# Kernel tuning notes

Hardware: AMD Instinct MI355X
Metric: run time of the kernel (lower is better)

The kernel has to match this reference:

```python
import jax, jax.numpy as jnp
import numpy as np

E4M3_MAX = 448.0
IGNORE = -1000.0
ROTARY_BASE = 10000.0


def quant_dequant_e4m3(w):
    """Emulate per-tensor FP8 E4M3 quantize->dequantize (3 mantissa bits, max 448)."""
    amax = jnp.max(jnp.abs(w))
    scale = E4M3_MAX / jnp.maximum(amax, 1e-12)
    v = w * scale
    a = jnp.abs(v)
    # exponent clipped to E4M3 range (min normal exp -6, max 8)
    e = jnp.clip(jnp.floor(jnp.log2(jnp.maximum(a, 1e-30))), -6.0, 8.0)
    step = jnp.exp2(e - 3.0)  # 3 mantissa bits
    q = jnp.clip(jnp.round(v / step) * step, -E4M3_MAX, E4M3_MAX)
    return (q / scale).astype(w.dtype)


def rotary_sin_cos(rotary_dim, n_ctx):
    pos = jnp.arange(n_ctx, dtype=jnp.float32)
    dim = jnp.arange(rotary_dim // 2, dtype=jnp.float32)
    inv_freq = ROTARY_BASE ** (-dim / (rotary_dim / 2))
    ang = pos[:, None] * inv_freq[None, :]            # [n_ctx, rotary_dim//2]
    ang = jnp.concatenate([ang, ang], axis=-1)        # [n_ctx, rotary_dim]
    return jnp.sin(ang), jnp.cos(ang)


def apply_rotary(x, sin, cos, rotary_dim):
    # x: [B, S, H, Dh]; rotate first rotary_dim dims with rotate-half convention
    S = x.shape[1]
    x_rot, x_pass = x[..., :rotary_dim], x[..., rotary_dim:]
    half = rotary_dim // 2
    x_flip = jnp.concatenate([-x_rot[..., half:], x_rot[..., :half]], axis=-1)
    c = cos[:S][None, :, None, :]
    s = sin[:S][None, :, None, :]
    out = x_rot * c + x_flip * s
    return jnp.concatenate([out, x_pass], axis=-1) if rotary_dim < x.shape[-1] else out


def setup_inputs() -> dict:
    key = jax.random.key(0)
    ks = jax.random.split(key, 8)
    B, S, D, H, Dh = 2, 2048, 1024, 16, 64
    return {
        "query_input": jax.random.normal(ks[0], (B, S, D), jnp.float32),
        "key_input": jax.random.normal(ks[1], (B, S, D), jnp.float32),
        "value_input": jax.random.normal(ks[2], (B, S, D), jnp.float32),
        "W_Q": jax.random.normal(ks[3], (H, D, Dh), jnp.float32) * 0.02,
        "W_K": jax.random.normal(ks[4], (H, D, Dh), jnp.float32) * 0.02,
        "W_V": jax.random.normal(ks[5], (H, D, Dh), jnp.float32) * 0.02,
        "W_O": jax.random.normal(ks[6], (H, Dh, D), jnp.float32) * 0.02,
        "b_Q": jnp.zeros((H, Dh), jnp.float32),
        "b_K": jnp.zeros((H, Dh), jnp.float32),
        "b_V": jnp.zeros((H, Dh), jnp.float32),
        "b_O": jnp.zeros((D,), jnp.float32),
    }


def reference(query_input, key_input, value_input, W_Q, W_K, W_V, W_O, b_Q, b_K, b_V, b_O):
    B, S, D = query_input.shape
    H, _, Dh = W_Q.shape
    rotary_dim = Dh
    attn_scale = jnp.sqrt(jnp.asarray(Dh, jnp.float32))

    # FP8-quantized QKV weights/biases (E4M3 quant-dequant emulation)
    Wq = quant_dequant_e4m3(W_Q)
    Wk = quant_dequant_e4m3(W_K)
    Wv = quant_dequant_e4m3(W_V)
    bq = quant_dequant_e4m3(b_Q)
    bk = quant_dequant_e4m3(b_K)
    bv = quant_dequant_e4m3(b_V)

    q = jnp.einsum("bsd,hde->bshe", query_input, Wq) + bq  # [B,S,H,Dh]
    k = jnp.einsum("bsd,hde->bshe", key_input, Wk) + bk
    v = jnp.einsum("bsd,hde->bshe", value_input, Wv) + bv

    sin, cos = rotary_sin_cos(rotary_dim, S)
    q = apply_rotary(q, sin, cos, rotary_dim)
    k = apply_rotary(k, sin, cos, rotary_dim)

    scores = jnp.einsum("bqhe,bkhe->bhqk", q, k) / attn_scale  # [B,H,S,S]
    causal = jnp.tril(jnp.ones((S, S), bool))
    scores = jnp.where(causal[None, None], scores, IGNORE)
    pattern = jax.nn.softmax(scores, axis=-1)

    z = jnp.einsum("bhqk,bkhe->bqhe", pattern, v)             # [B,S,H,Dh]
    out = jnp.einsum("bqhe,hed->bqd", z, W_O) + b_O           # [B,S,D]
    return out
```

## Files before the change

kernel.cpp:

```cpp
#include <hip/hip_runtime.h>
#include <math.h>


typedef __attribute__((ext_vector_type(8))) short bf16x8;
typedef __attribute__((ext_vector_type(16))) float f32x16;
typedef __attribute__((ext_vector_type(4))) float f32x4;
typedef __attribute__((ext_vector_type(4))) float f4;

#define E4M3_MAX 448.0f

__device__ inline float bf2f(ushort u) { return __uint_as_float(((unsigned)u) << 16); }
__device__ inline ushort f2bf(float f) {
  unsigned u = __float_as_uint(f);
  return (ushort)((u + 0x7FFF + ((u >> 16) & 1)) >> 16);
}
__device__ inline unsigned pack2bf(float a, float b) {
  unsigned ua = __float_as_uint(a), ub = __float_as_uint(b);
  return ((ua + 0x8000u) >> 16) | ((ub + 0x8000u) & 0xFFFF0000u);
}

__device__ __forceinline__ void gll16(const ushort* g, ushort* l) {
  __builtin_amdgcn_global_load_lds(
      (const __attribute__((address_space(1))) unsigned int*)g,
      (__attribute__((address_space(3))) unsigned int*)l, 16, 0, 0);
}

__global__ void zero16_kernel(float* p) {
  if (threadIdx.x < 16) p[threadIdx.x] = 0.0f;
}

__global__ __launch_bounds__(256) void amax6_kernel(const float* __restrict__ p0,
                                                    const float* __restrict__ p1,
                                                    const float* __restrict__ p2,
                                                    const float* __restrict__ p3,
                                                    const float* __restrict__ p4,
                                                    const float* __restrict__ p5,
                                                    float* __restrict__ amax) {
  int y = blockIdx.y;
  const float* src = (y == 0) ? p0 : (y == 1) ? p1 : (y == 2) ? p2 : (y == 3) ? p3 : (y == 4) ? p4 : p5;
  int n = (y < 3) ? 1048576 : 1024;
  float m = 0.0f;
  int stride = gridDim.x * 256;
  for (int i = blockIdx.x * 256 + threadIdx.x; i < n; i += stride)
    m = fmaxf(m, fabsf(src[i]));
  #pragma unroll
  for (int off = 32; off > 0; off >>= 1)
    m = fmaxf(m, __shfl_xor(m, off));
  __shared__ float wred[4];
  if ((threadIdx.x & 63) == 0) wred[threadIdx.x >> 6] = m;
  __syncthreads();
  if (threadIdx.x == 0) {
    m = fmaxf(fmaxf(wred[0], wred[1]), fmaxf(wred[2], wred[3]));
    atomicMax((unsigned int*)(amax + y), __float_as_uint(m));
  }
}

__device__ inline float qdq_qval(float w, float amax) {
  float scale = E4M3_MAX / fmaxf(amax, 1e-12f);
  float v = w * scale;
  float a = fmaxf(fabsf(v), 1e-30f);
  int ex;
  (void)frexpf(a, &ex);
  float e = fminf(fmaxf((float)(ex - 1), -6.0f), 8.0f);
  float step = exp2f(e - 3.0f);
  float q = rintf(v / step) * step;
  return fminf(fmaxf(q, -E4M3_MAX), E4M3_MAX);
}

__global__ void qvec3_kernel(const float* __restrict__ b0, const float* __restrict__ b1,
                             const float* __restrict__ b2, const float* __restrict__ amax,
                             float* __restrict__ o0, float* __restrict__ o1,
                             float* __restrict__ o2) {
  int y = blockIdx.y;
  const float* b = (y == 0) ? b0 : (y == 1) ? b1 : b2;
  float* o = (y == 0) ? o0 : (y == 1) ? o1 : o2;
  float am = amax[3 + y];
  int idx = blockIdx.x * blockDim.x + threadIdx.x;
  if (idx < 1024) {
    float q = qdq_qval(b[idx], am);
    o[idx] = q * (fmaxf(am, 1e-12f) * (1.0f / E4M3_MAX));
  }
}

__global__ __launch_bounds__(256) void quant_repack_bt3(const float* __restrict__ W0,
                                                        const float* __restrict__ W1,
                                                        const float* __restrict__ W2,
                                                        const float* __restrict__ amaxp,
                                                        ushort* __restrict__ o0,
                                                        ushort* __restrict__ o1,
                                                        ushort* __restrict__ o2) {
  int z = blockIdx.z;
  const float* W = (z == 0) ? W0 : (z == 1) ? W1 : W2;
  ushort* Bt = (z == 0) ? o0 : (z == 1) ? o1 : o2;
  float amax = amaxp[z];
  __shared__ float tile[64][65];
  int d0 = blockIdx.x * 64, hh = blockIdx.y;
  int tid = threadIdx.x;
  int e = tid & 63, dd = tid >> 6;
  #pragma unroll
  for (int p = 0; p < 16; p++)
    tile[dd + p * 4][e] = W[(size_t)hh * 65536 + (size_t)(d0 + dd + p * 4) * 64 + e];
  __syncthreads();
  int d = tid & 63, ee = tid >> 6;
  #pragma unroll
  for (int p = 0; p < 16; p++) {
    int e2 = ee + p * 4;
    Bt[(size_t)(hh * 64 + e2) * 1024 + d0 + d] = f2bf(qdq_qval(tile[d][e2], amax));
  }
}

__global__ __launch_bounds__(256) void wo_trans(const float* __restrict__ W,
                                               ushort* __restrict__ Bt) {
  __shared__ float tile[64][65];
  int d0 = blockIdx.x * 64, he0 = blockIdx.y * 64;
  int tid = threadIdx.x;
  int dcol = tid & 63, hr = tid >> 6;
  #pragma unroll
  for (int p = 0; p < 16; p++)
    tile[hr + p * 4][dcol] = W[(size_t)(he0 + hr + p * 4) * 1024 + d0 + dcol];
  __syncthreads();
  int hcol = tid & 63, dr = tid >> 6;
  #pragma unroll
  for (int p = 0; p < 16; p++)
    Bt[(size_t)(d0 + dr + p * 4) * 1024 + he0 + hcol] = f2bf(tile[hcol][dr + p * 4]);
}

__global__ __launch_bounds__(256) void cvt3_kernel(const float* __restrict__ i0,
                                                   const float* __restrict__ i1,
                                                   const float* __restrict__ i2,
                                                   ushort* __restrict__ o0,
                                                   ushort* __restrict__ o1,
                                                   ushort* __restrict__ o2) {
  int y = blockIdx.y;
  const float* in = (y == 0) ? i0 : (y == 1) ? i1 : i2;
  ushort* out = (y == 0) ? o0 : (y == 1) ? o1 : o2;
  int i = blockIdx.x * 256 + threadIdx.x;
  f4 v = *(const f4*)(in + (size_t)i * 4);
  uint2 o;
  o.x = (unsigned)f2bf(v[0]) | ((unsigned)f2bf(v[1]) << 16);
  o.y = (unsigned)f2bf(v[2]) | ((unsigned)f2bf(v[3]) << 16);
  *(uint2*)(out + (size_t)i * 4) = o;
}

template <int QUANT, int TN>
__device__ __forceinline__ void gemm_body(const ushort* __restrict__ A,
                                          const ushort* __restrict__ Bt,
                                          const float* __restrict__ bias, float s_inv,
                                          ushort* __restrict__ outb, float* __restrict__ outf,
                                          int bx, int by, ushort* As, ushort* Bs) {
  const int K = 1024, N = 1024;
  const int JF = TN / 32;
  int tid = threadIdx.x;
  int w = tid >> 6, lane = tid & 63, quad = lane >> 4, l16 = lane & 15;
  int wm = w & 1, wn = w >> 1;
  int row0 = by * 128, col0 = bx * TN;
  f32x4 acc[4][4] = {};

  for (int k0 = 0; k0 < K; k0 += 32) {
    __syncthreads();
    {
      int u = tid;
      gll16(&A[(size_t)(row0 + (u >> 2)) * K + k0 + (u & 3) * 8], &As[u * 8]);
      u = tid + 256;
      gll16(&A[(size_t)(row0 + (u >> 2)) * K + k0 + (u & 3) * 8], &As[u * 8]);
      u = tid;
      gll16(&Bt[(size_t)(col0 + (u >> 2)) * K + k0 + (u & 3) * 8], &Bs[u * 8]);
      if (TN == 128) {
        u = tid + 256;
        gll16(&Bt[(size_t)(col0 + (u >> 2)) * K + k0 + (u & 3) * 8], &Bs[u * 8]);
      }
    }
    __syncthreads();
    bf16x8 af[4], bfr[JF];
    #pragma unroll
    for (int i = 0; i < 4; i++)
      af[i] = *(const bf16x8*)&As[(wm * 64 + i * 16 + l16) * 32 + quad * 8];
    #pragma unroll
    for (int j = 0; j < JF; j++)
      bfr[j] = *(const bf16x8*)&Bs[(wn * (TN / 2) + j * 16 + l16) * 32 + quad * 8];
    #pragma unroll
    for (int i = 0; i < 4; i++)
      #pragma unroll
      for (int j = 0; j < JF; j++)
        acc[i][j] = __builtin_amdgcn_mfma_f32_16x16x32_bf16(af[i], bfr[j], acc[i][j], 0, 0, 0);
  }

  #pragma unroll
  for (int j = 0; j < JF; j++) {
    int col = col0 + wn * (TN / 2) + j * 16 + l16;
    float bv = bias[col];
    #pragma unroll
    for (int i = 0; i < 4; i++) {
      int row = row0 + wm * 64 + i * 16 + quad * 4;
      #pragma unroll
      for (int r = 0; r < 4; r++) {
        float v = acc[i][j][r] * s_inv + bv;
        if (QUANT) outb[(size_t)(row + r) * N + col] = f2bf(v);
        else       outf[(size_t)(row + r) * N + col] = v;
      }
    }
  }
}

__global__ __launch_bounds__(256) void gemm3_qkv(const ushort* __restrict__ xq,
                                                 const ushort* __restrict__ xk,
                                                 const ushort* __restrict__ xv,
                                                 const ushort* __restrict__ wq,
                                                 const ushort* __restrict__ wk,
                                                 const ushort* __restrict__ wv,
                                                 const float* __restrict__ bq,
                                                 const float* __restrict__ bk,
                                                 const float* __restrict__ bv,
                                                 const float* __restrict__ amax,
                                                 ushort* __restrict__ oq,
                                                 ushort* __restrict__ ok,
                                                 ushort* __restrict__ ov) {
  __shared__ ushort As[4096], Bs[4096];
  int z = blockIdx.z;
  const ushort* A  = (z == 0) ? xq : (z == 1) ? xk : xv;
  const ushort* Bt = (z == 0) ? wq : (z == 1) ? wk : wv;
  const float* bias = (z == 0) ? bq : (z == 1) ? bk : bv;
  ushort* out = (z == 0) ? oq : (z == 1) ? ok : ov;
  float s_inv = fmaxf(amax[z], 1e-12f) * (1.0f / E4M3_MAX);
  gemm_body<1, 128>(A, Bt, bias, s_inv, out, nullptr, blockIdx.x, blockIdx.y, As, Bs);
}

__global__ __launch_bounds__(256) void gemm_wo(const ushort* __restrict__ A,
                                               const ushort* __restrict__ Bt,
                                               const float* __restrict__ bias,
                                               float* __restrict__ out) {
  __shared__ ushort As[4096], Bs[2048];
  gemm_body<0, 64>(A, Bt, bias, 1.0f, nullptr, out, blockIdx.x, blockIdx.y, As, Bs);
}

__global__ __launch_bounds__(256) void rotary_bf(ushort* qb, ushort* kb) {
  int bs = blockIdx.x;
  int s = bs & 2047;
  int tid = threadIdx.x;
  int e = tid & 63, w = tid >> 6;
  int j = e & 31;
  float inv_freq = exp2f((float)j * (-13.287712379549449f / 32.0f));
  float ang = (float)s * inv_freq;
  float c = cosf(ang), sn = sinf(ang);
  float sgn = (e < 32) ? -1.0f : 1.0f;
  size_t base = (size_t)bs * 1024;
  #pragma unroll
  for (int i = 0; i < 4; i++) {
    int h = w + i * 4;
    size_t idx = base + (size_t)h * 64 + e;
    float x = bf2f(qb[idx]);
    float xp = __shfl_xor(x, 32);
    qb[idx] = f2bf(x * c + sgn * xp * sn);
    float y = bf2f(kb[idx]);
    float yp = __shfl_xor(y, 32);
    kb[idx] = f2bf(y * c + sgn * yp * sn);
  }
}

__global__ __launch_bounds__(256) void v_trans(const ushort* __restrict__ v,
                                              ushort* __restrict__ vT) {
  __shared__ ushort tile[64][72];
  int s0 = blockIdx.x * 64, h = blockIdx.y, b = blockIdx.z;
  int tid = threadIdx.x;
  int e = tid & 63, sr = tid >> 6;
  #pragma unroll
  for (int p = 0; p < 16; p++)
    tile[sr + p * 4][e] = v[(size_t)(b * 2048 + s0 + sr + p * 4) * 1024 + h * 64 + e];
  __syncthreads();
  int sc = tid & 63, er = tid >> 6;
  #pragma unroll
  for (int p = 0; p < 16; p++)
    vT[(size_t)((b * 16 + h) * 64 + er + p * 4) * 2048 + s0 + sc] = tile[sc][er + p * 4];
}

__global__ __launch_bounds__(512, 4) void flash_mfma6(const ushort* __restrict__ qb,
                                                      const ushort* __restrict__ kb,
                                                      const ushort* __restrict__ vT,
                                                      ushort* __restrict__ zb) {
  int h = blockIdx.y, b = blockIdx.z;
  int tid = threadIdx.x;
  int w8 = tid >> 6;
  int g = w8 >> 2;
  int w = w8 & 3;
  int lane = tid & 63, h2 = lane >> 5, l31 = lane & 31;
  __shared__ ushort sbuf[16384 + 18432];
  ushort* Ks = sbuf + g * 4096;
  ushort* Vs = sbuf + 8192 + g * 4096;
  ushort* P2 = sbuf + 16384 + g * 9216;

  const int qrow = w * 32 + l31;
  const float CE = 0.125f;

  const int ts = tid & 255;
  const int u0 = ts, u1 = ts + 256;
  const int r0 = u0 >> 3, c0 = u0 & 7, r1 = u1 >> 3, c1 = u1 & 7;
  const int sw0 = (c0 ^ (r0 & 7)) * 8, sw1 = (c1 ^ (r1 & 7)) * 8;

  #pragma unroll 1
  for (int rep = 0; rep < 2; rep++) {
    const int qt = (rep == 0) ? (15 - (int)blockIdx.x) : (int)blockIdx.x;
    const int q0 = qt * 128;
    const int qg = q0 + w * 32 + l31;
    size_t qbase = ((size_t)(b * 2048 + qg)) * 1024 + (size_t)h * 64;
    bf16x8 qf[4];
    #pragma unroll
    for (int ck = 0; ck < 4; ck++)
      qf[ck] = *(const bf16x8*)&qb[qbase + ck * 16 + h2 * 8];

    f32x16 accO[2] = {};
    float mrun = -INFINITY, lrun = 0.0f;

    const int nt = qt + 1;
    const int kt0 = g * nt;

    const ushort* ksrc0 = kb + ((size_t)(b * 2048 + kt0 * 64 + r0)) * 1024 + (size_t)h * 64 + c0 * 8;
    const ushort* ksrc1 = kb + ((size_t)(b * 2048 + kt0 * 64 + r1)) * 1024 + (size_t)h * 64 + c1 * 8;
    const ushort* vsrc0 = vT + ((size_t)((b * 16 + h) * 64 + r0)) * 2048 + kt0 * 64 + c0 * 8;
    const ushort* vsrc1 = vT + ((size_t)((b * 16 + h) * 64 + r1)) * 2048 + kt0 * 64 + c1 * 8;

    uint4 kc0 = *(const uint4*)ksrc0;
    uint4 kc1 = *(const uint4*)ksrc1;
    uint4 vc0 = *(const uint4*)vsrc0;
    uint4 vc1 = *(const uint4*)vsrc1;

    for (int t = 0; t < nt; t++) {
      int kt = kt0 + t;
      __syncthreads();
      *(uint4*)&Ks[r0 * 64 + sw0] = kc0;
      *(uint4*)&Ks[r1 * 64 + sw1] = kc1;
      *(uint4*)&Vs[r0 * 64 + sw0] = vc0;
      *(uint4*)&Vs[r1 * 64 + sw1] = vc1;
      __syncthreads();
      if (t + 1 < nt) {
        kc0 = *(const uint4*)(ksrc0 + (size_t)(t + 1) * 65536);
        kc1 = *(const uint4*)(ksrc1 + (size_t)(t + 1) * 65536);
        vc0 = *(const uint4*)(vsrc0 + (t + 1) * 64);
        vc1 = *(const uint4*)(vsrc1 + (t + 1) * 64);
      }

      bool active = (kt * 64 <= q0 + w * 32 + 31);
      if (active) {
        f32x16 sc[2] = {};
        #pragma unroll
        for (int mf = 0; mf < 2; mf++) {
          int row = mf * 32 + l31;
          int s8 = row & 7;
          #pragma unroll
          for (int ck = 0; ck < 4; ck++) {
            bf16x8 ka = *(const bf16x8*)&Ks[row * 64 + (((2 * ck + h2) ^ s8) * 8)];
            sc[mf] = __builtin_amdgcn_mfma_f32_32x32x16_bf16(ka, qf[ck], sc[mf], 0, 0, 0);
          }
        }

        if (kt * 64 + 63 > q0 + w * 32) {
          #pragma unroll
          for (int mf = 0; mf < 2; mf++)
            #pragma unroll
            for (int i = 0; i < 16; i++) {
              int kv = kt * 64 + mf * 32 + (i & 3) + 8 * (i >> 2) + 4 * h2;
              sc[mf][i] = (kv > qg) ? -8000.0f : sc[mf][i];
            }
        }

        float tm = sc[0][0];
        #pragma unroll
        for (int i = 1; i < 16; i++) tm = fmaxf(tm, sc[0][i]);
        #pragma unroll
        for (int i = 0; i < 16; i++) tm = fmaxf(tm, sc[1][i]);
        tm = fmaxf(tm, __shfl_xor(tm, 32));
        float mnew = fmaxf(mrun, tm);
        float alpha = __expf((mrun - mnew) * CE);
        float p[2][16];
        float rs = 0.0f;
        #pragma unroll
        for (int mf = 0; mf < 2; mf++)
          #pragma unroll
          for (int i = 0; i < 16; i++) {
            float pv = __expf((sc[mf][i] - mnew) * CE);
            p[mf][i] = pv;
            rs += pv;
          }
        rs += __shfl_xor(rs, 32);
        lrun = lrun * alpha + rs;
        mrun = mnew;
        #pragma unroll
        for (int mf = 0; mf < 2; mf++)
          #pragma unroll
          for (int i = 0; i < 16; i++) accO[mf][i] *= alpha;

        #pragma unroll
        for (int mf = 0; mf < 2; mf++)
          #pragma unroll
          for (int m = 0; m < 4; m++) {
            uint2 w2;
            w2.x = pack2bf(p[mf][4 * m + 0], p[mf][4 * m + 1]);
            w2.y = pack2bf(p[mf][4 * m + 2], p[mf][4 * m + 3]);
            *(uint2*)&P2[qrow * 72 + 32 * mf + 8 * m + 4 * h2] = w2;
          }

        #pragma unroll
        for (int ck = 0; ck < 4; ck++) {
          bf16x8 pB = *(const bf16x8*)&P2[qrow * 72 + ck * 16 + h2 * 8];
          #pragma unroll
          for (int mf = 0; mf < 2; mf++) {
            int row = mf * 32 + l31;
            bf16x8 va = *(const bf16x8*)&Vs[row * 64 + (((2 * ck + h2) ^ (row & 7)) * 8)];
            accO[mf] = __builtin_amdgcn_mfma_f32_32x32x16_bf16(va, pB, accO[mf], 0, 0, 0);
          }
        }
      }
    }

    __syncthreads();
    float* mbuf = (float*)sbuf;
    int midx = (w * 64 + lane) * 35;
    if (g == 1) {
      #pragma unroll
      for (int i = 0; i < 16; i++) mbuf[midx + i] = accO[0][i];
      #pragma unroll
      for (int i = 0; i < 16; i++) mbuf[midx + 16 + i] = accO[1][i];
      mbuf[midx + 32] = mrun;
      mbuf[midx + 33] = lrun;
    }
    __syncthreads();
    ushort* Osb = sbuf + 16384 + 9216;
    if (g == 0) {
      float m1 = mbuf[midx + 32], l1 = mbuf[midx + 33];
      float mn = fmaxf(mrun, m1);
      float a0 = __expf((mrun - mn) * CE), a1 = __expf((m1 - mn) * CE);
      float linv = 1.0f / (lrun * a0 + l1 * a1);
      #pragma unroll
      for (int mf = 0; mf < 2; mf++)
        #pragma unroll
        for (int m = 0; m < 4; m++) {
          int e0 = 32 * mf + 8 * m + 4 * h2;
          float o0 = (accO[mf][4 * m + 0] * a0 + mbuf[midx + 16 * mf + 4 * m + 0] * a1) * linv;
          float o1 = (accO[mf][4 * m + 1] * a0 + mbuf[midx + 16 * mf + 4 * m + 1] * a1) * linv;
          float o2 = (accO[mf][4 * m + 2] * a0 + mbuf[midx + 16 * mf + 4 * m + 2] * a1) * linv;
          float o3 = (accO[mf][4 * m + 3] * a0 + mbuf[midx + 16 * mf + 4 * m + 3] * a1) * linv;
          *(unsigned*)&Osb[qrow * 72 + e0] = pack2bf(o0, o1);
          *(unsigned*)&Osb[qrow * 72 + e0 + 2] = pack2bf(o2, o3);
        }
    }
    __syncthreads();
    size_t obase = ((size_t)(b * 2048 + q0)) * 1024 + (size_t)h * 64;
    #pragma unroll
    for (int i = 0; i < 2; i++) {
      int u = tid + i * 512;
      int r = u >> 3, blk = u & 7;
      *(uint4*)&zb[obase + (size_t)r * 1024 + blk * 8] = *(const uint4*)&Osb[r * 72 + blk * 8];
    }
  }
}

extern "C" void kernel_launch(void* const* d_in, const int* in_sizes, int n_in,
                              void* d_out, int out_size, void* d_ws, size_t ws_size,
                              hipStream_t stream) {
  const float* Xq  = (const float*)d_in[0];
  const float* Xk  = (const float*)d_in[1];
  const float* Xv  = (const float*)d_in[2];
  const float* W_Q = (const float*)d_in[3];
  const float* W_K = (const float*)d_in[4];
  const float* W_V = (const float*)d_in[5];
  const float* W_O = (const float*)d_in[6];
  const float* b_Q = (const float*)d_in[7];
  const float* b_K = (const float*)d_in[8];
  const float* b_V = (const float*)d_in[9];
  const float* b_O = (const float*)d_in[10];
  float* out = (float*)d_out;

  char* base = (char*)d_ws;
  float*  amax = (float*)(base + 0);
  float*  bq   = (float*)(base + 4096);
  float*  bk   = (float*)(base + 8192);
  float*  bv   = (float*)(base + 12288);
  ushort* wq   = (ushort*)(base + 16384);
  ushort* wk   = (ushort*)(base + 16384 + 2097152);
  ushort* wv   = (ushort*)(base + 16384 + 2u * 2097152);
  ushort* woT  = (ushort*)(base + 16384 + 3u * 2097152);
  ushort* xq   = (ushort*)(base + 8404992);
  ushort* xk   = (ushort*)(base + 16793600);
  ushort* xv   = (ushort*)(base + 25182208);
  ushort* qbf  = (ushort*)(base + 33570816);
  ushort* kbf  = (ushort*)(base + 41959424);
  ushort* vbf  = (ushort*)(base + 50348032);
  ushort* vT   = xq;
  ushort* zbf  = xk;

  zero16_kernel<<<1, 64, 0, stream>>>(amax);
  dim3 agrid(64, 6);
  amax6_kernel<<<agrid, 256, 0, stream>>>(W_Q, W_K, W_V, b_Q, b_K, b_V, amax);

  dim3 rgrid(16, 16, 3);
  quant_repack_bt3<<<rgrid, 256, 0, stream>>>(W_Q, W_K, W_V, amax, wq, wk, wv);
  dim3 qvgrid(4, 3);
  qvec3_kernel<<<qvgrid, 256, 0, stream>>>(b_Q, b_K, b_V, amax, bq, bk, bv);
  dim3 wgrid(16, 16);
  wo_trans<<<wgrid, 256, 0, stream>>>(W_O, woT);
  dim3 cgrid(4096, 3);
  cvt3_kernel<<<cgrid, 256, 0, stream>>>(Xq, Xk, Xv, xq, xk, xv);

  dim3 g3(8, 32, 3);
  gemm3_qkv<<<g3, 256, 0, stream>>>(xq, xk, xv, wq, wk, wv, bq, bk, bv, amax,
                                    qbf, kbf, vbf);

  rotary_bf<<<4096, 256, 0, stream>>>(qbf, kbf);

  dim3 vgrid(32, 16, 2);
  v_trans<<<vgrid, 16 * 16, 0, stream>>>(vbf, vT);

  dim3 fgrid(8, 16, 2);
  flash_mfma6<<<fgrid, 512, 0, stream>>>(qbf, kbf, vT, zbf);

  dim3 wog(16, 32);
  gemm_wo<<<wog, 256, 0, stream>>>(zbf, woT, b_O, out);
}
```

Measured before the change: 270.5 us.

## Split flash attention KV range across four wave groups per block

Blocks of the flash attention kernel grow from 512 to 1024 threads, and the KV tiles for each query tile are split across four groups of waves instead of two, with an uneven remainder spread across groups. Partial outputs and softmax statistics from groups 1 to 3 are merged through shared memory into group 0. The aim is more parallelism per query tile and a shorter serial KV loop, which helps the long causal rows. The cost is more shared memory (about 136KB), lower occupancy, and extra barrier iterations for groups that have fewer tiles.

```diff
diff --git a/kernel.cpp b/kernel.cpp
--- a/kernel.cpp
+++ b/kernel.cpp
@@ -273,20 +273,19 @@
     vT[(size_t)((b * 16 + h) * 64 + er + p * 4) * 2048 + s0 + sc] = tile[sc][er + p * 4];
 }
 
-__global__ __launch_bounds__(512, 4) void flash_mfma6(const ushort* __restrict__ qb,
-                                                      const ushort* __restrict__ kb,
-                                                      const ushort* __restrict__ vT,
-                                                      ushort* __restrict__ zb) {
+__global__ __launch_bounds__(1024, 4) void flash_mfma7(const ushort* __restrict__ qb,
+                                                       const ushort* __restrict__ kb,
+                                                       const ushort* __restrict__ vT,
+                                                       ushort* __restrict__ zb) {
   int h = blockIdx.y, b = blockIdx.z;
   int tid = threadIdx.x;
-  int w8 = tid >> 6;
-  int g = w8 >> 2;
-  int w = w8 & 3;
+  int g = tid >> 8;
+  int w = (tid >> 6) & 3;
   int lane = tid & 63, h2 = lane >> 5, l31 = lane & 31;
-  __shared__ ushort sbuf[16384 + 18432];
+  __shared__ ushort sbuf[69632];
   ushort* Ks = sbuf + g * 4096;
-  ushort* Vs = sbuf + 8192 + g * 4096;
-  ushort* P2 = sbuf + 16384 + g * 9216;
+  ushort* Vs = sbuf + 16384 + g * 4096;
+  ushort* P2 = sbuf + 32768 + g * 9216;
 
   const int qrow = w * 32 + l31;
   const float CE = 0.125f;
@@ -310,8 +309,11 @@
     f32x16 accO[2] = {};
     float mrun = -INFINITY, lrun = 0.0f;
 
-    const int nt = qt + 1;
-    const int kt0 = g * nt;
+    const int T = 2 * qt + 2;
+    const int qd = T >> 2, rr = T & 3;
+    const int nt = qd + (g < rr ? 1 : 0);
+    const int kt0 = g * qd + (g < rr ? g : rr);
+    const int ntmax = qd + (rr ? 1 : 0);
 
     const ushort* ksrc0 = kb + ((size_t)(b * 2048 + kt0 * 64 + r0)) * 1024 + (size_t)h * 64 + c0 * 8;
     const ushort* ksrc1 = kb + ((size_t)(b * 2048 + kt0 * 64 + r1)) * 1024 + (size_t)h * 64 + c1 * 8;
@@ -323,7 +325,7 @@
     uint4 vc0 = *(const uint4*)vsrc0;
     uint4 vc1 = *(const uint4*)vsrc1;
 
-    for (int t = 0; t < nt; t++) {
+    for (int t = 0; t < ntmax; t++) {
       int kt = kt0 + t;
       __syncthreads();
       *(uint4*)&Ks[r0 * 64 + sw0] = kc0;
@@ -338,7 +340,7 @@
         vc1 = *(const uint4*)(vsrc1 + (t + 1) * 64);
       }
 
-      bool active = (kt * 64 <= q0 + w * 32 + 31);
+      bool active = (t < nt) && (kt * 64 <= q0 + w * 32 + 31);
       if (active) {
         f32x16 sc[2] = {};
         #pragma unroll
@@ -413,8 +415,8 @@
 
     __syncthreads();
     float* mbuf = (float*)sbuf;
-    int midx = (w * 64 + lane) * 35;
-    if (g == 1) {
+    if (g > 0) {
+      int midx = ((g - 1) * 256 + w * 64 + lane) * 35;
       #pragma unroll
       for (int i = 0; i < 16; i++) mbuf[midx + i] = accO[0][i];
       #pragma unroll
@@ -423,30 +425,36 @@
       mbuf[midx + 33] = lrun;
     }
     __syncthreads();
-    ushort* Osb = sbuf + 16384 + 9216;
+    ushort* Osb = sbuf + 53760;
     if (g == 0) {
-      float m1 = mbuf[midx + 32], l1 = mbuf[midx + 33];
-      float mn = fmaxf(mrun, m1);
+      int i1 = (w * 64 + lane) * 35;
+      int i2 = (256 + w * 64 + lane) * 35;
+      int i3 = (512 + w * 64 + lane) * 35;
+      float m1 = mbuf[i1 + 32], l1 = mbuf[i1 + 33];
+      float m2 = mbuf[i2 + 32], l2 = mbuf[i2 + 33];
+      float m3 = mbuf[i3 + 32], l3 = mbuf[i3 + 33];
+      float mn = fmaxf(fmaxf(mrun, m1), fmaxf(m2, m3));
       float a0 = __expf((mrun - mn) * CE), a1 = __expf((m1 - mn) * CE);
-      float linv = 1.0f / (lrun * a0 + l1 * a1);
+      float a2 = __expf((m2 - mn) * CE), a3 = __expf((m3 - mn) * CE);
+      float linv = 1.0f / (lrun * a0 + l1 * a1 + l2 * a2 + l3 * a3);
       #pragma unroll
       for (int mf = 0; mf < 2; mf++)
         #pragma unroll
         for (int m = 0; m < 4; m++) {
+          int idx = 16 * mf + 4 * m;
           int e0 = 32 * mf + 8 * m + 4 * h2;
-          float o0 = (accO[mf][4 * m + 0] * a0 + mbuf[midx + 16 * mf + 4 * m + 0] * a1) * linv;
-          float o1 = (accO[mf][4 * m + 1] * a0 + mbuf[midx + 16 * mf + 4 * m + 1] * a1) * linv;
-          float o2 = (accO[mf][4 * m + 2] * a0 + mbuf[midx + 16 * mf + 4 * m + 2] * a1) * linv;
-          float o3 = (accO[mf][4 * m + 3] * a0 + mbuf[midx + 16 * mf + 4 * m + 3] * a1) * linv;
+          float o0 = (accO[mf][4 * m + 0] * a0 + mbuf[i1 + idx + 0] * a1 + mbuf[i2 + idx + 0] * a2 + mbuf[i3 + idx + 0] * a3) * linv;
+          float o1 = (accO[mf][4 * m + 1] * a0 + mbuf[i1 + idx + 1] * a1 + mbuf[i2 + idx + 1] * a2 + mbuf[i3 + idx + 1] * a3) * linv;
+          float o2 = (accO[mf][4 * m + 2] * a0 + mbuf[i1 + idx + 2] * a1 + mbuf[i2 + idx + 2] * a2 + mbuf[i3 + idx + 2] * a3) * linv;
+          float o3 = (accO[mf][4 * m + 3] * a0 + mbuf[i1 + idx + 3] * a1 + mbuf[i2 + idx + 3] * a2 + mbuf[i3 + idx + 3] * a3) * linv;
           *(unsigned*)&Osb[qrow * 72 + e0] = pack2bf(o0, o1);
           *(unsigned*)&Osb[qrow * 72 + e0 + 2] = pack2bf(o2, o3);
         }
     }
     __syncthreads();
     size_t obase = ((size_t)(b * 2048 + q0)) * 1024 + (size_t)h * 64;
-    #pragma unroll
-    for (int i = 0; i < 2; i++) {
-      int u = tid + i * 512;
+    {
+      int u = tid;
       int r = u >> 3, blk = u & 7;
       *(uint4*)&zb[obase + (size_t)r * 1024 + blk * 8] = *(const uint4*)&Osb[r * 72 + blk * 8];
     }
@@ -510,7 +518,7 @@
   v_trans<<<vgrid, 16 * 16, 0, stream>>>(vbf, vT);
 
   dim3 fgrid(8, 16, 2);
-  flash_mfma6<<<fgrid, 512, 0, stream>>>(qbf, kbf, vT, zbf);
+  flash_mfma7<<<fgrid, 1024, 0, stream>>>(qbf, kbf, vT, zbf);
 
   dim3 wog(16, 32);
   gemm_wo<<<wog, 256, 0, stream>>>(zbf, woT, b_O, out);
```

New measurement: 278.8 us. +3.1%, slower.

## Merge preprocessing and rotary/V-transpose kernels into fewer launches

Applied to the files above, without the earlier changes.

Replaces the atomic-based amax reduction with per-block partial maxima that are reduced inside the consumer kernel. This removes the zeroing kernel and the atomics. The weight quantization, bias quantization, W_O transpose and input conversion are packed into two combined launches, and rotary and the V transpose are merged into one launch. The aim is to cut launch count and serialization gaps between small kernels. The cost is redundant 64-element reductions in every consumer block.

```diff
diff --git a/kernel.cpp b/kernel.cpp
--- a/kernel.cpp
+++ b/kernel.cpp
@@ -23,36 +23,6 @@
   __builtin_amdgcn_global_load_lds(
       (const __attribute__((address_space(1))) unsigned int*)g,
       (__attribute__((address_space(3))) unsigned int*)l, 16, 0, 0);
-}
-
-__global__ void zero16_kernel(float* p) {
-  if (threadIdx.x < 16) p[threadIdx.x] = 0.0f;
-}
-
-__global__ __launch_bounds__(256) void amax6_kernel(const float* __restrict__ p0,
-                                                    const float* __restrict__ p1,
-                                                    const float* __restrict__ p2,
-                                                    const float* __restrict__ p3,
-                                                    const float* __restrict__ p4,
-                                                    const float* __restrict__ p5,
-                                                    float* __restrict__ amax) {
-  int y = blockIdx.y;
-  const float* src = (y == 0) ? p0 : (y == 1) ? p1 : (y == 2) ? p2 : (y == 3) ? p3 : (y == 4) ? p4 : p5;
-  int n = (y < 3) ? 1048576 : 1024;
-  float m = 0.0f;
-  int stride = gridDim.x * 256;
-  for (int i = blockIdx.x * 256 + threadIdx.x; i < n; i += stride)
-    m = fmaxf(m, fabsf(src[i]));
-  #pragma unroll
-  for (int off = 32; off > 0; off >>= 1)
-    m = fmaxf(m, __shfl_xor(m, off));
-  __shared__ float wred[4];
-  if ((threadIdx.x & 63) == 0) wred[threadIdx.x >> 6] = m;
-  __syncthreads();
-  if (threadIdx.x == 0) {
-    m = fmaxf(fmaxf(wred[0], wred[1]), fmaxf(wred[2], wred[3]));
-    atomicMax((unsigned int*)(amax + y), __float_as_uint(m));
-  }
 }
 
 __device__ inline float qdq_qval(float w, float amax) {
@@ -67,79 +37,117 @@
   return fminf(fmaxf(q, -E4M3_MAX), E4M3_MAX);
 }
 
-__global__ void qvec3_kernel(const float* __restrict__ b0, const float* __restrict__ b1,
-                             const float* __restrict__ b2, const float* __restrict__ amax,
-                             float* __restrict__ o0, float* __restrict__ o1,
-                             float* __restrict__ o2) {
-  int y = blockIdx.y;
-  const float* b = (y == 0) ? b0 : (y == 1) ? b1 : b2;
-  float* o = (y == 0) ? o0 : (y == 1) ? o1 : o2;
-  float am = amax[3 + y];
-  int idx = blockIdx.x * blockDim.x + threadIdx.x;
-  if (idx < 1024) {
-    float q = qdq_qval(b[idx], am);
-    o[idx] = q * (fmaxf(am, 1e-12f) * (1.0f / E4M3_MAX));
+__device__ __forceinline__ float redpart64(const float* __restrict__ p, int tid) {
+  float v = p[tid & 63];
+  #pragma unroll
+  for (int o = 32; o > 0; o >>= 1) v = fmaxf(v, __shfl_xor(v, o));
+  return v;
+}
+
+__global__ __launch_bounds__(256) void prep1(const float* __restrict__ W0,
+                                             const float* __restrict__ W1,
+                                             const float* __restrict__ W2,
+                                             const float* __restrict__ b0,
+                                             const float* __restrict__ b1,
+                                             const float* __restrict__ b2,
+                                             const float* __restrict__ Xq,
+                                             const float* __restrict__ Xk,
+                                             const float* __restrict__ Xv,
+                                             float* __restrict__ amaxpart,
+                                             ushort* __restrict__ xq,
+                                             ushort* __restrict__ xk,
+                                             ushort* __restrict__ xv) {
+  __shared__ float wred[4];
+  int bid = blockIdx.x, tid = threadIdx.x;
+  if (bid < 384) {
+    int y = bid >> 6, xb = bid & 63;
+    const float* src = (y == 0) ? W0 : (y == 1) ? W1 : (y == 2) ? W2
+                     : (y == 3) ? b0 : (y == 4) ? b1 : b2;
+    int n = (y < 3) ? 1048576 : 1024;
+    float m = 0.0f;
+    for (int i = xb * 256 + tid; i < n; i += 64 * 256)
+      m = fmaxf(m, fabsf(src[i]));
+    #pragma unroll
+    for (int off = 32; off > 0; off >>= 1)
+      m = fmaxf(m, __shfl_xor(m, off));
+    if ((tid & 63) == 0) wred[tid >> 6] = m;
+    __syncthreads();
+    if (tid == 0)
+      amaxpart[y * 64 + xb] = fmaxf(fmaxf(wred[0], wred[1]), fmaxf(wred[2], wred[3]));
+  } else {
+    int t = bid - 384;
+    int y = t >> 12, xb = t & 4095;
+    const float* in = (y == 0) ? Xq : (y == 1) ? Xk : Xv;
+    ushort* out = (y == 0) ? xq : (y == 1) ? xk : xv;
+    int i = xb * 256 + tid;
+    f4 v = *(const f4*)(in + (size_t)i * 4);
+    uint2 o;
+    o.x = (unsigned)f2bf(v[0]) | ((unsigned)f2bf(v[1]) << 16);
+    o.y = (unsigned)f2bf(v[2]) | ((unsigned)f2bf(v[3]) << 16);
+    *(uint2*)(out + (size_t)i * 4) = o;
   }
 }
 
-__global__ __launch_bounds__(256) void quant_repack_bt3(const float* __restrict__ W0,
-                                                        const float* __restrict__ W1,
-                                                        const float* __restrict__ W2,
-                                                        const float* __restrict__ amaxp,
-                                                        ushort* __restrict__ o0,
-                                                        ushort* __restrict__ o1,
-                                                        ushort* __restrict__ o2) {
-  int z = blockIdx.z;
-  const float* W = (z == 0) ? W0 : (z == 1) ? W1 : W2;
-  ushort* Bt = (z == 0) ? o0 : (z == 1) ? o1 : o2;
-  float amax = amaxp[z];
+__global__ __launch_bounds__(256) void prep2(const float* __restrict__ W0,
+                                             const float* __restrict__ W1,
+                                             const float* __restrict__ W2,
+                                             const float* __restrict__ WO,
+                                             const float* __restrict__ b0,
+                                             const float* __restrict__ b1,
+                                             const float* __restrict__ b2,
+                                             const float* __restrict__ amaxpart,
+                                             float* __restrict__ amax,
+                                             ushort* __restrict__ o0,
+                                             ushort* __restrict__ o1,
+                                             ushort* __restrict__ o2,
+                                             ushort* __restrict__ woT,
+                                             float* __restrict__ bq,
+                                             float* __restrict__ bk,
+                                             float* __restrict__ bv) {
   __shared__ float tile[64][65];
-  int d0 = blockIdx.x * 64, hh = blockIdx.y;
-  int tid = threadIdx.x;
-  int e = tid & 63, dd = tid >> 6;
-  #pragma unroll
-  for (int p = 0; p < 16; p++)
-    tile[dd + p * 4][e] = W[(size_t)hh * 65536 + (size_t)(d0 + dd + p * 4) * 64 + e];
-  __syncthreads();
-  int d = tid & 63, ee = tid >> 6;
-  #pragma unroll
-  for (int p = 0; p < 16; p++) {
-    int e2 = ee + p * 4;
-    Bt[(size_t)(hh * 64 + e2) * 1024 + d0 + d] = f2bf(qdq_qval(tile[d][e2], amax));
+  int bid = blockIdx.x, tid = threadIdx.x;
+  if (bid < 768) {
+    int z = bid >> 8, r = bid & 255, hh = r >> 4, xb = r & 15;
+    const float* W = (z == 0) ? W0 : (z == 1) ? W1 : W2;
+    ushort* Bt = (z == 0) ? o0 : (z == 1) ? o1 : o2;
+    float am = redpart64(amaxpart + z * 64, tid);
+    if (r == 0 && tid == 0) amax[z] = am;
+    int d0 = xb * 64;
+    int e = tid & 63, dd = tid >> 6;
+    #pragma unroll
+    for (int p = 0; p < 16; p++)
+      tile[dd + p * 4][e] = W[(size_t)hh * 65536 + (size_t)(d0 + dd + p * 4) * 64 + e];
+    __syncthreads();
+    int d = tid & 63, ee = tid >> 6;
+    #pragma unroll
+    for (int p = 0; p < 16; p++) {
+      int e2 = ee + p * 4;
+      Bt[(size_t)(hh * 64 + e2) * 1024 + d0 + d] = f2bf(qdq_qval(tile[d][e2], am));
+    }
+  } else if (bid < 780) {
+    int q = bid - 768, y = q >> 2, xb = q & 3;
+    const float* b = (y == 0) ? b0 : (y == 1) ? b1 : b2;
+    float* o = (y == 0) ? bq : (y == 1) ? bk : bv;
+    float am = redpart64(amaxpart + (3 + y) * 64, tid);
+    int idx = xb * 256 + tid;
+    if (idx < 1024) {
+      float qv = qdq_qval(b[idx], am);
+      o[idx] = qv * (fmaxf(am, 1e-12f) * (1.0f / E4M3_MAX));
+    }
+  } else {
+    int t = bid - 780;
+    int xb = t & 15, yb = t >> 4;
+    int d0 = xb * 64, he0 = yb * 64;
+    int dcol = tid & 63, hr = tid >> 6;
+    #pragma unroll
+    for (int p = 0; p < 16; p++)
+      tile[hr + p * 4][dcol] = WO[(size_t)(he0 + hr + p * 4) * 1024 + d0 + dcol];
+    __syncthreads();
+    int hcol = tid & 63, dr = tid >> 6;
+    #pragma unroll
+    for (int p = 0; p < 16; p++)
+      woT[(size_t)(d0 + dr + p * 4) * 1024 + he0 + hcol] = f2bf(tile[hcol][dr + p * 4]);
   }
-}
-
-__global__ __launch_bounds__(256) void wo_trans(const float* __restrict__ W,
-                                               ushort* __restrict__ Bt) {
-  __shared__ float tile[64][65];
-  int d0 = blockIdx.x * 64, he0 = blockIdx.y * 64;
-  int tid = threadIdx.x;
-  int dcol = tid & 63, hr = tid >> 6;
-  #pragma unroll
-  for (int p = 0; p < 16; p++)
-    tile[hr + p * 4][dcol] = W[(size_t)(he0 + hr + p * 4) * 1024 + d0 + dcol];
-  __syncthreads();
-  int hcol = tid & 63, dr = tid >> 6;
-  #pragma unroll
-  for (int p = 0; p < 16; p++)
-    Bt[(size_t)(d0 + dr + p * 4) * 1024 + he0 + hcol] = f2bf(tile[hcol][dr + p * 4]);
-}
-
-__global__ __launch_bounds__(256) void cvt3_kernel(const float* __restrict__ i0,
-                                                   const float* __restrict__ i1,
-                                                   const float* __restrict__ i2,
-                                                   ushort* __restrict__ o0,
-                                                   ushort* __restrict__ o1,
-                                                   ushort* __restrict__ o2) {
-  int y = blockIdx.y;
-  const float* in = (y == 0) ? i0 : (y == 1) ? i1 : i2;
-  ushort* out = (y == 0) ? o0 : (y == 1) ? o1 : o2;
-  int i = blockIdx.x * 256 + threadIdx.x;
-  f4 v = *(const f4*)(in + (size_t)i * 4);
-  uint2 o;
-  o.x = (unsigned)f2bf(v[0]) | ((unsigned)f2bf(v[1]) << 16);
-  o.y = (unsigned)f2bf(v[2]) | ((unsigned)f2bf(v[3]) << 16);
-  *(uint2*)(out + (size_t)i * 4) = o;
 }
 
 template <int QUANT, int TN>
@@ -233,44 +241,47 @@
   gemm_body<0, 64>(A, Bt, bias, 1.0f, nullptr, out, blockIdx.x, blockIdx.y, As, Bs);
 }
 
-__global__ __launch_bounds__(256) void rotary_bf(ushort* qb, ushort* kb) {
-  int bs = blockIdx.x;
-  int s = bs & 2047;
-  int tid = threadIdx.x;
-  int e = tid & 63, w = tid >> 6;
-  int j = e & 31;
-  float inv_freq = exp2f((float)j * (-13.287712379549449f / 32.0f));
-  float ang = (float)s * inv_freq;
-  float c = cosf(ang), sn = sinf(ang);
-  float sgn = (e < 32) ? -1.0f : 1.0f;
-  size_t base = (size_t)bs * 1024;
-  #pragma unroll
-  for (int i = 0; i < 4; i++) {
-    int h = w + i * 4;
-    size_t idx = base + (size_t)h * 64 + e;
-    float x = bf2f(qb[idx]);
-    float xp = __shfl_xor(x, 32);
-    qb[idx] = f2bf(x * c + sgn * xp * sn);
-    float y = bf2f(kb[idx]);
-    float yp = __shfl_xor(y, 32);
-    kb[idx] = f2bf(y * c + sgn * yp * sn);
+__global__ __launch_bounds__(256) void rot_vtrans(ushort* __restrict__ qb,
+                                                  ushort* __restrict__ kb,
+                                                  const ushort* __restrict__ v,
+                                                  ushort* __restrict__ vT) {
+  __shared__ ushort tile[64][72];
+  int bid = blockIdx.x, tid = threadIdx.x;
+  if (bid < 4096) {
+    int bs = bid;
+    int s = bs & 2047;
+    int e = tid & 63, w = tid >> 6;
+    int j = e & 31;
+    float inv_freq = exp2f((float)j * (-13.287712379549449f / 32.0f));
+    float ang = (float)s * inv_freq;
+    float c = cosf(ang), sn = sinf(ang);
+    float sgn = (e < 32) ? -1.0f : 1.0f;
+    size_t base = (size_t)bs * 1024;
+    #pragma unroll
+    for (int i = 0; i < 4; i++) {
+      int h = w + i * 4;
+      size_t idx = base + (size_t)h * 64 + e;
+      float x = bf2f(qb[idx]);
+      float xp = __shfl_xor(x, 32);
+      qb[idx] = f2bf(x * c + sgn * xp * sn);
+      float y = bf2f(kb[idx]);
+      float yp = __shfl_xor(y, 32);
+      kb[idx] = f2bf(y * c + sgn * yp * sn);
+    }
+  } else {
+    int t = bid - 4096;
+    int sx = t & 31, h = (t >> 5) & 15, b = t >> 9;
+    int s0 = sx * 64;
+    int e = tid & 63, sr = tid >> 6;
+    #pragma unroll
+    for (int p = 0; p < 16; p++)
+      tile[sr + p * 4][e] = v[(size_t)(b * 2048 + s0 + sr + p * 4) * 1024 + h * 64 + e];
+    __syncthreads();
+    int sc = tid & 63, er = tid >> 6;
+    #pragma unroll
+    for (int p = 0; p < 16; p++)
+      vT[(size_t)((b * 16 + h) * 64 + er + p * 4) * 2048 + s0 + sc] = tile[sc][er + p * 4];
   }
-}
-
-__global__ __launch_bounds__(256) void v_trans(const ushort* __restrict__ v,
-                                              ushort* __restrict__ vT) {
-  __shared__ ushort tile[64][72];
-  int s0 = blockIdx.x * 64, h = blockIdx.y, b = blockIdx.z;
-  int tid = threadIdx.x;
-  int e = tid & 63, sr = tid >> 6;
-  #pragma unroll
-  for (int p = 0; p < 16; p++)
-    tile[sr + p * 4][e] = v[(size_t)(b * 2048 + s0 + sr + p * 4) * 1024 + h * 64 + e];
-  __syncthreads();
-  int sc = tid & 63, er = tid >> 6;
-  #pragma unroll
-  for (int p = 0; p < 16; p++)
-    vT[(size_t)((b * 16 + h) * 64 + er + p * 4) * 2048 + s0 + sc] = tile[sc][er + p * 4];
 }
 
 __global__ __launch_bounds__(512, 4) void flash_mfma6(const ushort* __restrict__ qb,
@@ -471,6 +482,7 @@
 
   char* base = (char*)d_ws;
   float*  amax = (float*)(base + 0);
+  float*  amaxpart = (float*)(base + 1024);
   float*  bq   = (float*)(base + 4096);
   float*  bk   = (float*)(base + 8192);
   float*  bv   = (float*)(base + 12288);
@@ -487,31 +499,16 @@
   ushort* vT   = xq;
   ushort* zbf  = xk;
 
-  zero16_kernel<<<1, 64, 0, stream>>>(amax);
-  dim3 agrid(64, 6);
-  amax6_kernel<<<agrid, 256, 0, stream>>>(W_Q, W_K, W_V, b_Q, b_K, b_V, amax);
-
-  dim3 rgrid(16, 16, 3);
-  quant_repack_bt3<<<rgrid, 256, 0, stream>>>(W_Q, W_K, W_V, amax, wq, wk, wv);
-  dim3 qvgrid(4, 3);
-  qvec3_kernel<<<qvgrid, 256, 0, stream>>>(b_Q, b_K, b_V, amax, bq, bk, bv);
-  dim3 wgrid(16, 16);
-  wo_trans<<<wgrid, 256, 0, stream>>>(W_O, woT);
-  dim3 cgrid(4096, 3);
-  cvt3_kernel<<<cgrid, 256, 0, stream>>>(Xq, Xk, Xv, xq, xk, xv);
-
+  prep1<<<12672, 256, 0, stream>>>(W_Q, W_K, W_V, b_Q, b_K, b_V, Xq, Xk, Xv,
+                                   amaxpart, xq, xk, xv);
+  prep2<<<1036, 256, 0, stream>>>(W_Q, W_K, W_V, W_O, b_Q, b_K, b_V,
+                                  amaxpart, amax, wq, wk, wv, woT, bq, bk, bv);
   dim3 g3(8, 32, 3);
   gemm3_qkv<<<g3, 256, 0, stream>>>(xq, xk, xv, wq, wk, wv, bq, bk, bv, amax,
                                     qbf, kbf, vbf);
-
-  rotary_bf<<<4096, 256, 0, stream>>>(qbf, kbf);
-
-  dim3 vgrid(32, 16, 2);
-  v_trans<<<vgrid, 16 * 16, 0, stream>>>(vbf, vT);
-
+  rot_vtrans<<<5120, 256, 0, stream>>>(qbf, kbf, vbf, vT);
   dim3 fgrid(8, 16, 2);
   flash_mfma6<<<fgrid, 512, 0, stream>>>(qbf, kbf, vT, zbf);
-
   dim3 wog(16, 32);
   gemm_wo<<<wog, 256, 0, stream>>>(zbf, woT, b_O, out);
 }
```

Result: faster. 253.5 us (-6.3%).
